# Performance work log

Hardware: AMD Instinct MI355X
Metric: run time of the kernel (lower is better)

The kernel has to match this reference:

```python
import jax, jax.numpy as jnp
import numpy as np

B, N, M = 2, 2048, 1024
C, CTX, H = 1024, 1024, 16
D = C // H
HID = int(C * 4.0)
EPS = 1e-6


def _ln(h):
    # LayerNorm32: fp32 layernorm, eps=1e-6, no affine params
    h32 = h.astype(jnp.float32)
    mu = jnp.mean(h32, axis=-1, keepdims=True)
    var = jnp.var(h32, axis=-1, keepdims=True)
    return ((h32 - mu) * jax.lax.rsqrt(var + EPS)).astype(h.dtype)


def _sdpa(q, k, v):
    # q: [B,Q,H,D], k/v: [B,K,H,D]
    scale = 1.0 / np.sqrt(D)
    s = jnp.einsum('bqhd,bkhd->bhqk', q, k) * scale
    p = jax.nn.softmax(s, axis=-1)
    return jnp.einsum('bhqk,bkhd->bqhd', p, v)


def _forward(x, context, Wqkv, bqkv, Wos, bos, Wq, bq, Wkv, bkv, Woc, boc, W1, b1, W2, b2):
    Bx, Nx, _ = x.shape
    Mx = context.shape[1]
    # --- self-attention (attn_mode='full') ---
    h = _ln(x)
    qkv = (h @ Wqkv + bqkv).reshape(Bx, Nx, 3, H, D)
    q, k, v = qkv[:, :, 0], qkv[:, :, 1], qkv[:, :, 2]
    a = _sdpa(q, k, v).reshape(Bx, Nx, C)
    x = x + (a @ Wos + bos)
    # --- cross-attention (always 'full') ---
    h = _ln(x)
    q = (h @ Wq + bq).reshape(Bx, Nx, H, D)
    kv = (context @ Wkv + bkv).reshape(Bx, Mx, 2, H, D)
    k, v = kv[:, :, 0], kv[:, :, 1]
    a = _sdpa(q, k, v).reshape(Bx, Nx, C)
    x = x + (a @ Woc + boc)
    # --- FFN with tanh-approx GELU ---
    h = _ln(x)
    x = x + (jax.nn.gelu(h @ W1 + b1, approximate=True) @ W2 + b2)
    return x


def setup_inputs() -> dict:
    key = jax.random.key(0)
    ks = jax.random.split(key, 12)
    rn = lambda k, shape: (jax.random.normal(k, shape, jnp.float32) * 0.02)
    return {
        'x': jax.random.normal(ks[0], (B, N, C), jnp.float32),
        'context': jax.random.normal(ks[1], (B, M, CTX), jnp.float32),
        'Wqkv': rn(ks[2], (C, 3 * C)), 'bqkv': jnp.zeros((3 * C,), jnp.float32),
        'Wos': rn(ks[3], (C, C)), 'bos': jnp.zeros((C,), jnp.float32),
        'Wq': rn(ks[4], (C, C)), 'bq': jnp.zeros((C,), jnp.float32),
        'Wkv': rn(ks[5], (CTX, 2 * C)), 'bkv': jnp.zeros((2 * C,), jnp.float32),
        'Woc': rn(ks[6], (C, C)), 'boc': jnp.zeros((C,), jnp.float32),
        'W1': rn(ks[7], (C, HID)), 'b1': jnp.zeros((HID,), jnp.float32),
        'W2': rn(ks[8], (HID, C)), 'b2': jnp.zeros((C,), jnp.float32),
    }


def reference(x, context, Wqkv, bqkv, Wos, bos, Wq, bq, Wkv, bkv, Woc, boc, W1, b1, W2, b2):
    return _forward(x, context, Wqkv, bqkv, Wos, bos, Wq, bq, Wkv, bkv, Woc, boc, W1, b1, W2, b2)
```

## Files before the change

### kernel.cpp

```cpp
#include <hip/hip_runtime.h>
#include <cstdint>

typedef unsigned short u16;
typedef short bf16x8 __attribute__((ext_vector_type(8)));
typedef unsigned short u16x8 __attribute__((ext_vector_type(8)));
typedef float f32x4 __attribute__((ext_vector_type(4)));

__device__ __forceinline__ u16 f2bf(float f) {
  union { float f; uint32_t u; } v; v.f = f;
  uint32_t r = (v.u + 0x7fffu + ((v.u >> 16) & 1u)) >> 16;
  return (u16)r;
}

__device__ __forceinline__ void gload_lds16(const u16* g, u16* l) {
  __builtin_amdgcn_global_load_lds(
      (const __attribute__((address_space(1))) void*)g,
      (__attribute__((address_space(3))) void*)l, 16, 0, 0);
}

__global__ __launch_bounds__(256) void ln_kernel(const float* __restrict__ x,
                                                 u16* __restrict__ h) {
  const int row = blockIdx.x;
  const int tid = threadIdx.x;
  const float4 v = *reinterpret_cast<const float4*>(x + (long)row * 1024 + tid * 4);
  float s  = v.x + v.y + v.z + v.w;
  float ss = v.x * v.x + v.y * v.y + v.z * v.z + v.w * v.w;
#pragma unroll
  for (int off = 32; off >= 1; off >>= 1) {
    s  += __shfl_xor(s, off, 64);
    ss += __shfl_xor(ss, off, 64);
  }
  __shared__ float red[8];
  const int wave = tid >> 6, lane = tid & 63;
  if (lane == 0) { red[wave] = s; red[4 + wave] = ss; }
  __syncthreads();
  s  = red[0] + red[1] + red[2] + red[3];
  ss = red[4] + red[5] + red[6] + red[7];
  const float mu   = s * (1.0f / 1024.0f);
  const float var  = ss * (1.0f / 1024.0f) - mu * mu;
  const float rstd = rsqrtf(var + 1e-6f);
  ushort4 o;
  o.x = f2bf((v.x - mu) * rstd);
  o.y = f2bf((v.y - mu) * rstd);
  o.z = f2bf((v.z - mu) * rstd);
  o.w = f2bf((v.w - mu) * rstd);
  *reinterpret_cast<ushort4*>(h + (long)row * 1024 + tid * 4) = o;
}

struct WEnt { const float* W; u16* Wt; int K, N, tEnd; };
struct WEnts { WEnt e[7]; int n; };

__global__ __launch_bounds__(256) void wconvert_all(WEnts args) {
  __shared__ u16 tile[64][72];
  int t = blockIdx.x;
  int i = 0, tStart = 0;
  while (i < args.n - 1 && t >= args.e[i].tEnd) { tStart = args.e[i].tEnd; i++; }
  const float* W = args.e[i].W;
  u16* Wt = args.e[i].Wt;
  const int K = args.e[i].K, N = args.e[i].N;
  const int rel = t - tStart;
  const int ntn = N >> 6;
  const int tn = rel % ntn, tk = rel / ntn;
  const int n0 = tn * 64, k0 = tk * 64;

  const int th = threadIdx.x;
  const int c4 = (th & 15) * 4;
  const int r  = th >> 4;
#pragma unroll
  for (int ii = 0; ii < 4; ii++) {
    const int row = ii * 16 + r;
    const float4 v = *reinterpret_cast<const float4*>(W + (long)(k0 + row) * N + n0 + c4);
    tile[c4 + 0][row] = f2bf(v.x);
    tile[c4 + 1][row] = f2bf(v.y);
    tile[c4 + 2][row] = f2bf(v.z);
    tile[c4 + 3][row] = f2bf(v.w);
  }
  __syncthreads();
  const int c8 = (th & 7) * 8;
  const int rn = th >> 3;
#pragma unroll
  for (int ii = 0; ii < 2; ii++) {
    const int row = ii * 32 + rn;
    *reinterpret_cast<u16x8*>(Wt + (long)(n0 + row) * K + k0 + c8) =
        *reinterpret_cast<const u16x8*>(&tile[row][c8]);
  }
}

__global__ __launch_bounds__(256) void f2bf_kernel(const float* __restrict__ in,
                                                   u16* __restrict__ out) {
  const long i = ((long)blockIdx.x * 256 + threadIdx.x) * 4;
  const float4 v = *reinterpret_cast<const float4*>(in + i);
  ushort4 o;
  o.x = f2bf(v.x); o.y = f2bf(v.y); o.z = f2bf(v.z); o.w = f2bf(v.w);
  *reinterpret_cast<ushort4*>(out + i) = o;
}

__global__ __launch_bounds__(256) void vtrans(const u16* __restrict__ V,
                                              u16* __restrict__ Vt,
                                              int vStride, long vBatch, int nk) {
  const int tid = threadIdx.x;
  const int b = blockIdx.z, h = blockIdx.y, n0 = blockIdx.x * 64;
  const u16* vp = V + (long)b * vBatch + h * 64;
  u16* op = Vt + (long)(b * 16 + h) * 64 * (long)nk + n0;
  const int d = tid >> 3;
  const int seg = tid & 7;
#pragma unroll
  for (int i = 0; i < 2; i++) {
    const int dd = i * 32 + d;
    u16x8 w;
#pragma unroll
    for (int j = 0; j < 8; j++) w[j] = vp[(long)(n0 + seg * 8 + j) * vStride + dd];
    *reinterpret_cast<u16x8*>(op + (long)dd * nk + seg * 8) = w;
  }
}

template <int TN, bool OUT_BF16, bool GELU_ACT, bool RES>
__global__ __launch_bounds__(256, 2) void gemm_bt(
    const u16* __restrict__ A, const u16* __restrict__ Bt,
    const float* __restrict__ bias, const float* __restrict__ res,
    void* __restrict__ Cout, int Ndim, int Kdim) {
  constexpr int NFRAG = TN / 32;
  __shared__ u16 Al[128 * 32];
  __shared__ u16 Bl[TN * 32];
  const int tid  = threadIdx.x;
  const int lane = tid & 63, wave = tid >> 6;
  const int quad = lane >> 4, l15 = lane & 15;
  const int wr = wave >> 1, wc = wave & 1;
  const int m0 = blockIdx.y * 128, n0 = blockIdx.x * TN;

  f32x4 acc[4][NFRAG];
  const f32x4 vzero = {0.f, 0.f, 0.f, 0.f};
#pragma unroll
  for (int i = 0; i < 4; i++)
#pragma unroll
    for (int j = 0; j < NFRAG; j++) acc[i][j] = vzero;

  const long rowOff = (long)(lane >> 2) * Kdim + (lane & 3) * 8;
  const u16* gA = A  + (long)m0 * Kdim + rowOff;
  const u16* gB = Bt + (long)n0 * Kdim + rowOff;

  for (int k0 = 0; k0 < Kdim; k0 += 32) {
    __syncthreads();
    gload_lds16(gA + (long)(wave * 16) * Kdim + k0,       &Al[wave * 512]);
    gload_lds16(gA + (long)((wave + 4) * 16) * Kdim + k0, &Al[(wave + 4) * 512]);
    gload_lds16(gB + (long)(wave * 16) * Kdim + k0,       &Bl[wave * 512]);
    if constexpr (TN == 128)
      gload_lds16(gB + (long)((wave + 4) * 16) * Kdim + k0, &Bl[(wave + 4) * 512]);
    __syncthreads();

    bf16x8 af[4], bfr[NFRAG];
#pragma unroll
    for (int mt = 0; mt < 4; mt++)
      af[mt] = *reinterpret_cast<const bf16x8*>(&Al[(wr * 64 + mt * 16 + l15) * 32 + quad * 8]);
#pragma unroll
    for (int nt = 0; nt < NFRAG; nt++)
      bfr[nt] = *reinterpret_cast<const bf16x8*>(&Bl[(wc * NFRAG * 16 + nt * 16 + l15) * 32 + quad * 8]);
#pragma unroll
    for (int mt = 0; mt < 4; mt++)
#pragma unroll
      for (int nt = 0; nt < NFRAG; nt++)
        acc[mt][nt] = __builtin_amdgcn_mfma_f32_16x16x32_bf16(af[mt], bfr[nt], acc[mt][nt], 0, 0, 0);
  }

#pragma unroll
  for (int nt = 0; nt < NFRAG; nt++) {
    const int col = n0 + wc * NFRAG * 16 + nt * 16 + l15;
    const float bv = bias[col];
#pragma unroll
    for (int mt = 0; mt < 4; mt++) {
#pragma unroll
      for (int r = 0; r < 4; r++) {
        const int row = m0 + wr * 64 + mt * 16 + quad * 4 + r;
        float y = acc[mt][nt][r] + bv;
        if (GELU_ACT) {
          const float t = 0.7978845608028654f * (y + 0.044715f * y * y * y);
          y = 0.5f * y * (1.0f + tanhf(t));
        }
        if (RES) y += res[(long)row * Ndim + col];
        if (OUT_BF16)
          ((u16*)Cout)[(long)row * Ndim + col] = f2bf(y);
        else
          ((float*)Cout)[(long)row * Ndim + col] = y;
      }
    }
  }
}

__global__ __launch_bounds__(256, 2) void attn_kernel(
    const u16* __restrict__ Q, const u16* __restrict__ K, const u16* __restrict__ Vt,
    u16* __restrict__ O, int nk, int qStride, int kStride, int oStride,
    long qBatch, long kBatch, long oBatch) {
  __shared__ u16 Kt[64 * 64];
  __shared__ u16 Vl[64 * 64];
  __shared__ u16 Pl[4][32 * 64];

  const int tid = threadIdx.x;
  const int lane = tid & 63, wave = tid >> 6;
  const int quad = lane >> 4, l15 = lane & 15;
  const int b = blockIdx.z, hh = blockIdx.y, qt = blockIdx.x;

  const u16* qp = Q + (long)b * qBatch + hh * 64;
  const u16* kp = K + (long)b * kBatch + hh * 64;
  const u16* vp = Vt + (long)(b * 16 + hh) * 64 * (long)nk;

  bf16x8 qf[2][2];
  const int qrow = qt * 128 + wave * 32 + l15;
#pragma unroll
  for (int qg = 0; qg < 2; qg++) {
    qf[qg][0] = *reinterpret_cast<const bf16x8*>(qp + (long)(qrow + qg * 16) * qStride + quad * 8);
    qf[qg][1] = *reinterpret_cast<const bf16x8*>(qp + (long)(qrow + qg * 16) * qStride + 32 + quad * 8);
  }

  const int r8 = lane >> 3;
  const int gcol = ((lane & 7) ^ r8) * 8;
  const u16* kgA = kp + (long)(wave * 8 + r8) * kStride + gcol;
  const u16* kgB = kp + (long)((wave + 4) * 8 + r8) * kStride + gcol;
  const u16* vgA = vp + (long)(wave * 8 + r8) * nk + gcol;
  const u16* vgB = vp + (long)((wave + 4) * 8 + r8) * nk + gcol;

  const int cF = (quad ^ (l15 & 7)) * 8;

  const f32x4 vzero = {0.f, 0.f, 0.f, 0.f};
  f32x4 oAcc[2][4];
  float lSt[2] = {0.f, 0.f};
#pragma unroll
  for (int qg = 0; qg < 2; qg++)
#pragma unroll
    for (int i = 0; i < 4; i++) oAcc[qg][i] = vzero;

  const float SCL = 0.18033688f;
  const int nTiles = nk >> 6;
  const long kAdv = (long)64 * kStride;

  for (int kt = 0; kt < nTiles; kt++) {
    __syncthreads();
    gload_lds16(kgA + kt * kAdv, &Kt[wave * 512]);
    gload_lds16(kgB + kt * kAdv, &Kt[(wave + 4) * 512]);
    gload_lds16(vgA + kt * 64,   &Vl[wave * 512]);
    gload_lds16(vgB + kt * 64,   &Vl[(wave + 4) * 512]);
    __syncthreads();

    f32x4 st[2][4];
#pragma unroll
    for (int mt = 0; mt < 4; mt++) {
      const bf16x8 kf0 = *reinterpret_cast<const bf16x8*>(&Kt[(mt * 16 + l15) * 64 + cF]);
      const bf16x8 kf1 = *reinterpret_cast<const bf16x8*>(&Kt[(mt * 16 + l15) * 64 + (cF ^ 32)]);
#pragma unroll
      for (int qg = 0; qg < 2; qg++) {
        f32x4 z = vzero;
        z = __builtin_amdgcn_mfma_f32_16x16x32_bf16(kf0, qf[qg][0], z, 0, 0, 0);
        z = __builtin_amdgcn_mfma_f32_16x16x32_bf16(kf1, qf[qg][1], z, 0, 0, 0);
        st[qg][mt] = z;
      }
    }

#pragma unroll
    for (int qg = 0; qg < 2; qg++) {
      float ps = 0.f;
#pragma unroll
      for (int mt = 0; mt < 4; mt++)
#pragma unroll
        for (int r = 0; r < 4; r++) {
          const float p = __builtin_amdgcn_exp2f(st[qg][mt][r] * SCL);
          st[qg][mt][r] = p;
          ps += p;
        }
      lSt[qg] += ps;
      u16* plw = &Pl[wave][(qg * 16 + l15) * 64];
#pragma unroll
      for (int mt = 0; mt < 4; mt++) {
        union { float f; uint32_t u; } a0, a1, a2, a3;
        a0.f = st[qg][mt][0]; a1.f = st[qg][mt][1];
        a2.f = st[qg][mt][2]; a3.f = st[qg][mt][3];
        a0.u += 0x8000u; a1.u += 0x8000u; a2.u += 0x8000u; a3.u += 0x8000u;
        uint2 w;
        w.x = __builtin_amdgcn_perm(a1.u, a0.u, 0x07060302u);
        w.y = __builtin_amdgcn_perm(a3.u, a2.u, 0x07060302u);
        const int pcol = (((mt * 2 + (quad >> 1)) ^ (l15 & 7)) * 8) + (quad & 1) * 4;
        *reinterpret_cast<uint2*>(&plw[pcol]) = w;
      }
    }

    bf16x8 pf[2][2];
#pragma unroll
    for (int qg = 0; qg < 2; qg++) {
      const u16* plw = &Pl[wave][(qg * 16 + l15) * 64];
      pf[qg][0] = *reinterpret_cast<const bf16x8*>(&plw[cF]);
      pf[qg][1] = *reinterpret_cast<const bf16x8*>(&plw[cF ^ 32]);
    }
#pragma unroll
    for (int dt = 0; dt < 4; dt++) {
      const bf16x8 vf0 = *reinterpret_cast<const bf16x8*>(&Vl[(dt * 16 + l15) * 64 + cF]);
      const bf16x8 vf1 = *reinterpret_cast<const bf16x8*>(&Vl[(dt * 16 + l15) * 64 + (cF ^ 32)]);
#pragma unroll
      for (int qg = 0; qg < 2; qg++) {
        oAcc[qg][dt] = __builtin_amdgcn_mfma_f32_16x16x32_bf16(pf[qg][0], vf0, oAcc[qg][dt], 0, 0, 0);
        oAcc[qg][dt] = __builtin_amdgcn_mfma_f32_16x16x32_bf16(pf[qg][1], vf1, oAcc[qg][dt], 0, 0, 0);
      }
    }
  }

  u16* op = O + (long)b * oBatch + hh * 64;
#pragma unroll
  for (int qg = 0; qg < 2; qg++) {
    float l = lSt[qg];
    l += __shfl_xor(l, 16, 64);
    l += __shfl_xor(l, 32, 64);
    float lR[4];
#pragma unroll
    for (int r = 0; r < 4; r++) lR[r] = 1.0f / __shfl(l, quad * 4 + r, 64);
#pragma unroll
    for (int dt = 0; dt < 4; dt++)
#pragma unroll
      for (int r = 0; r < 4; r++) {
        const int row = qt * 128 + wave * 32 + qg * 16 + quad * 4 + r;
        op[(long)row * oStride + dt * 16 + l15] = f2bf(oAcc[qg][dt][r] * lR[r]);
      }
  }
}

extern "C" void kernel_launch(void* const* d_in, const int* in_sizes, int n_in,
                              void* d_out, int out_size, void* d_ws, size_t ws_size,
                              hipStream_t stream) {
  const float* x    = (const float*)d_in[0];
  const float* ctx  = (const float*)d_in[1];
  const float* Wqkv = (const float*)d_in[2];
  const float* bqkv = (const float*)d_in[3];
  const float* Wos  = (const float*)d_in[4];
  const float* bos  = (const float*)d_in[5];
  const float* Wq   = (const float*)d_in[6];
  const float* bq   = (const float*)d_in[7];
  const float* Wkv  = (const float*)d_in[8];
  const float* bkv  = (const float*)d_in[9];
  const float* Woc  = (const float*)d_in[10];
  const float* boc  = (const float*)d_in[11];
  const float* W1   = (const float*)d_in[12];
  const float* b1   = (const float*)d_in[13];
  const float* W2   = (const float*)d_in[14];
  const float* b2   = (const float*)d_in[15];
  float* out = (float*)d_out;
  char* ws = (char*)d_ws;
  const size_t MB = 1024 * 1024;

  if (ws_size >= 80 * MB) {
    u16* Wqkvt = (u16*)(ws + 0 * MB);
    u16* Wost  = (u16*)(ws + 6 * MB);
    u16* Wqt   = (u16*)(ws + 8 * MB);
    u16* Wkvt  = (u16*)(ws + 10 * MB);
    u16* Woct  = (u16*)(ws + 14 * MB);
    u16* W1t   = (u16*)(ws + 16 * MB);
    u16* W2t   = (u16*)(ws + 24 * MB);
    u16* h     = (u16*)(ws + 32 * MB);
    u16* abuf  = (u16*)(ws + 40 * MB);
    u16* qkv   = (u16*)(ws + 48 * MB);
    u16* q2    = (u16*)(ws + 48 * MB);
    u16* kv2   = (u16*)(ws + 56 * MB);
    u16* ctxbf = (u16*)(ws + 64 * MB);
    u16* VtCr  = (u16*)(ws + 68 * MB);
    u16* hid   = (u16*)(ws + 48 * MB);
    u16* VtSelf = h;

    WEnts we;
    we.n = 7;
    we.e[0] = {Wqkv, Wqkvt, 1024, 3072, 768};
    we.e[1] = {Wos,  Wost,  1024, 1024, 1024};
    we.e[2] = {Wq,   Wqt,   1024, 1024, 1280};
    we.e[3] = {Wkv,  Wkvt,  1024, 2048, 1792};
    we.e[4] = {Woc,  Woct,  1024, 1024, 2048};
    we.e[5] = {W1,   W1t,   1024, 4096, 3072};
    we.e[6] = {W2,   W2t,   4096, 1024, 4096};
    wconvert_all<<<dim3(4096), dim3(256), 0, stream>>>(we);
    f2bf_kernel<<<dim3(2048), dim3(256), 0, stream>>>(ctx, ctxbf);

    ln_kernel<<<dim3(4096), dim3(256), 0, stream>>>(x, h);
    gemm_bt<128, true, false, false><<<dim3(24, 32), dim3(256), 0, stream>>>(
        h, Wqkvt, bqkv, nullptr, qkv, 3072, 1024);
    vtrans<<<dim3(32, 16, 2), dim3(256), 0, stream>>>(
        qkv + 2048, VtSelf, 3072, (long)2048 * 3072, 2048);
    attn_kernel<<<dim3(16, 16, 2), dim3(256), 0, stream>>>(
        qkv, qkv + 1024, VtSelf, abuf, 2048, 3072, 3072, 1024,
        (long)2048 * 3072, (long)2048 * 3072, (long)2048 * 1024);
    gemm_bt<64, false, false, true><<<dim3(16, 32), dim3(256), 0, stream>>>(
        abuf, Wost, bos, x, out, 1024, 1024);
    ln_kernel<<<dim3(4096), dim3(256), 0, stream>>>(out, h);
    gemm_bt<64, true, false, false><<<dim3(16, 32), dim3(256), 0, stream>>>(
        h, Wqt, bq, nullptr, q2, 1024, 1024);
    gemm_bt<64, true, false, false><<<dim3(32, 16), dim3(256), 0, stream>>>(
        ctxbf, Wkvt, bkv, nullptr, kv2, 2048, 1024);
    vtrans<<<dim3(16, 16, 2), dim3(256), 0, stream>>>(
        kv2 + 1024, VtCr, 2048, (long)1024 * 2048, 1024);
    attn_kernel<<<dim3(16, 16, 2), dim3(256), 0, stream>>>(
        q2, kv2, VtCr, abuf, 1024, 1024, 2048, 1024,
        (long)2048 * 1024, (long)1024 * 2048, (long)2048 * 1024);
    gemm_bt<64, false, false, true><<<dim3(16, 32), dim3(256), 0, stream>>>(
        abuf, Woct, boc, out, out, 1024, 1024);
    ln_kernel<<<dim3(4096), dim3(256), 0, stream>>>(out, h);
    gemm_bt<128, true, true, false><<<dim3(32, 32), dim3(256), 0, stream>>>(
        h, W1t, b1, nullptr, hid, 4096, 1024);
    gemm_bt<64, false, false, true><<<dim3(16, 32), dim3(256), 0, stream>>>(
        hid, W2t, b2, out, out, 1024, 4096);
  } else {
    u16* h      = (u16*)ws;
    u16* wbuf   = (u16*)(ws + 8 * MB);
    char* C0    = ws + 16 * MB;
    u16* qkv    = (u16*)C0;
    u16* Wqkvt  = (u16*)(C0 + 24 * MB);
    u16* Wost   = (u16*)C0;
    u16* q2     = (u16*)C0;
    u16* kv2    = (u16*)(C0 + 8 * MB);
    u16* Wqt    = (u16*)(C0 + 16 * MB);
    u16* Wkvt   = (u16*)(C0 + 16 * MB);
    u16* ctxbf  = (u16*)(C0 + 20 * MB);
    u16* VtCr   = (u16*)(C0 + 24 * MB);
    u16* Woct   = (u16*)(C0 + 16 * MB);
    u16* hid    = (u16*)C0;
    u16* VtSelf = h;
    u16* abuf   = wbuf;
    u16* W1t    = wbuf;
    u16* W2t    = wbuf;
    WEnts w1; w1.n = 1;

    ln_kernel<<<dim3(4096), dim3(256), 0, stream>>>(x, h);
    w1.e[0] = {Wqkv, Wqkvt, 1024, 3072, 768};
    wconvert_all<<<dim3(768), dim3(256), 0, stream>>>(w1);
    gemm_bt<128, true, false, false><<<dim3(24, 32), dim3(256), 0, stream>>>(
        h, Wqkvt, bqkv, nullptr, qkv, 3072, 1024);
    vtrans<<<dim3(32, 16, 2), dim3(256), 0, stream>>>(
        qkv + 2048, VtSelf, 3072, (long)2048 * 3072, 2048);
    attn_kernel<<<dim3(16, 16, 2), dim3(256), 0, stream>>>(
        qkv, qkv + 1024, VtSelf, abuf, 2048, 3072, 3072, 1024,
        (long)2048 * 3072, (long)2048 * 3072, (long)2048 * 1024);
    w1.e[0] = {Wos, Wost, 1024, 1024, 256};
    wconvert_all<<<dim3(256), dim3(256), 0, stream>>>(w1);
    gemm_bt<64, false, false, true><<<dim3(16, 32), dim3(256), 0, stream>>>(
        abuf, Wost, bos, x, out, 1024, 1024);
    ln_kernel<<<dim3(4096), dim3(256), 0, stream>>>(out, h);
    w1.e[0] = {Wq, Wqt, 1024, 1024, 256};
    wconvert_all<<<dim3(256), dim3(256), 0, stream>>>(w1);
    gemm_bt<64, true, false, false><<<dim3(16, 32), dim3(256), 0, stream>>>(
        h, Wqt, bq, nullptr, q2, 1024, 1024);
    f2bf_kernel<<<dim3(2048), dim3(256), 0, stream>>>(ctx, ctxbf);
    w1.e[0] = {Wkv, Wkvt, 1024, 2048, 512};
    wconvert_all<<<dim3(512), dim3(256), 0, stream>>>(w1);
    gemm_bt<64, true, false, false><<<dim3(32, 16), dim3(256), 0, stream>>>(
        ctxbf, Wkvt, bkv, nullptr, kv2, 2048, 1024);
    vtrans<<<dim3(16, 16, 2), dim3(256), 0, stream>>>(
        kv2 + 1024, VtCr, 2048, (long)1024 * 2048, 1024);
    attn_kernel<<<dim3(16, 16, 2), dim3(256), 0, stream>>>(
        q2, kv2, VtCr, abuf, 1024, 1024, 2048, 1024,
        (long)2048 * 1024, (long)1024 * 2048, (long)2048 * 1024);
    w1.e[0] = {Woc, Woct, 1024, 1024, 256};
    wconvert_all<<<dim3(256), dim3(256), 0, stream>>>(w1);
    gemm_bt<64, false, false, true><<<dim3(16, 32), dim3(256), 0, stream>>>(
        abuf, Woct, boc, out, out, 1024, 1024);
    ln_kernel<<<dim3(4096), dim3(256), 0, stream>>>(out, h);
    w1.e[0] = {W1, W1t, 1024, 4096, 1024};
    wconvert_all<<<dim3(1024), dim3(256), 0, stream>>>(w1);
    gemm_bt<128, true, true, false><<<dim3(32, 32), dim3(256), 0, stream>>>(
        h, W1t, b1, nullptr, hid, 4096, 1024);
    w1.e[0] = {W2, W2t, 4096, 1024, 1024};
    wconvert_all<<<dim3(1024), dim3(256), 0, stream>>>(w1);
    gemm_bt<64, false, false, true><<<dim3(16, 32), dim3(256), 0, stream>>>(
        hid, W2t, b2, out, out, 1024, 4096);
  }
}
```

Baseline: 508.6 us.

## Remap GEMM blocks to XCD-local tile groups and transpose V through LDS

The GEMM grid becomes 1D, and block indices are remapped so that each of the 8 XCDs (blocks assigned round-robin by j&7) gets a contiguous 2D region of output tiles. Neighbouring tiles then share A/B panels in that XCD's L2. The V transpose kernel now uses coalesced 16-byte row loads into an LDS tile and 16-byte stores, replacing strided scalar gathers. The price is extra index arithmetic, and correctness depends on the lx/ly/SX parameters exactly tiling each grid.

```diff
diff --git a/kernel.cpp b/kernel.cpp
--- a/kernel.cpp
+++ b/kernel.cpp
@@ -98,42 +98,54 @@
 __global__ __launch_bounds__(256) void vtrans(const u16* __restrict__ V,
                                               u16* __restrict__ Vt,
                                               int vStride, long vBatch, int nk) {
-  const int tid = threadIdx.x;
+  __shared__ u16 tile[64][72];
+  const int t = threadIdx.x;
   const int b = blockIdx.z, h = blockIdx.y, n0 = blockIdx.x * 64;
   const u16* vp = V + (long)b * vBatch + h * 64;
   u16* op = Vt + (long)(b * 16 + h) * 64 * (long)nk + n0;
-  const int d = tid >> 3;
-  const int seg = tid & 7;
+  const int ch = t & 7;
 #pragma unroll
   for (int i = 0; i < 2; i++) {
-    const int dd = i * 32 + d;
-    u16x8 w;
-#pragma unroll
-    for (int j = 0; j < 8; j++) w[j] = vp[(long)(n0 + seg * 8 + j) * vStride + dd];
-    *reinterpret_cast<u16x8*>(op + (long)dd * nk + seg * 8) = w;
-  }
-}
-
-template <int TN, bool OUT_BF16, bool GELU_ACT, bool RES>
+    const int n = (t >> 3) + i * 32;
+    const u16x8 v = *reinterpret_cast<const u16x8*>(vp + (long)(n0 + n) * vStride + ch * 8);
+#pragma unroll
+    for (int j = 0; j < 8; j++) tile[ch * 8 + j][n] = v[j];
+  }
+  __syncthreads();
+#pragma unroll
+  for (int i = 0; i < 2; i++) {
+    const int d = (t >> 3) + i * 32;
+    *reinterpret_cast<u16x8*>(op + (long)d * nk + ch * 8) =
+        *reinterpret_cast<const u16x8*>(&tile[d][ch * 8]);
+  }
+}
+
+template <int TN, int SX, bool OUT_BF16, bool GELU_ACT, bool RES>
 __global__ __launch_bounds__(256, 2) void gemm_bt(
     const u16* __restrict__ A, const u16* __restrict__ Bt,
     const float* __restrict__ bias, const float* __restrict__ res,
-    void* __restrict__ Cout, int Ndim, int Kdim) {
+    void* __restrict__ Cout, int Ndim, int Kdim, int lx, int ly) {
   constexpr int NFRAG = TN / 32;
   __shared__ u16 Al[128 * 32];
   __shared__ u16 Bl[TN * 32];
+  const int j = blockIdx.x;
+  const int c = j & 7, kk = j >> 3;
+  const int cx = c % SX, cy = c / SX;
+  const int bx = cx * lx + (kk % lx);
+  const int by = cy * ly + (kk / lx);
+  const int m0 = by * 128, n0 = bx * TN;
+
   const int tid  = threadIdx.x;
   const int lane = tid & 63, wave = tid >> 6;
   const int quad = lane >> 4, l15 = lane & 15;
   const int wr = wave >> 1, wc = wave & 1;
-  const int m0 = blockIdx.y * 128, n0 = blockIdx.x * TN;
 
   f32x4 acc[4][NFRAG];
   const f32x4 vzero = {0.f, 0.f, 0.f, 0.f};
 #pragma unroll
   for (int i = 0; i < 4; i++)
 #pragma unroll
-    for (int j = 0; j < NFRAG; j++) acc[i][j] = vzero;
+    for (int jj = 0; jj < NFRAG; jj++) acc[i][jj] = vzero;
 
   const long rowOff = (long)(lane >> 2) * Kdim + (lane & 3) * 8;
   const u16* gA = A  + (long)m0 * Kdim + rowOff;
@@ -373,32 +385,32 @@
     f2bf_kernel<<<dim3(2048), dim3(256), 0, stream>>>(ctx, ctxbf);
 
     ln_kernel<<<dim3(4096), dim3(256), 0, stream>>>(x, h);
-    gemm_bt<128, true, false, false><<<dim3(24, 32), dim3(256), 0, stream>>>(
-        h, Wqkvt, bqkv, nullptr, qkv, 3072, 1024);
+    gemm_bt<128, 2, true, false, false><<<dim3(768), dim3(256), 0, stream>>>(
+        h, Wqkvt, bqkv, nullptr, qkv, 3072, 1024, 12, 8);
     vtrans<<<dim3(32, 16, 2), dim3(256), 0, stream>>>(
         qkv + 2048, VtSelf, 3072, (long)2048 * 3072, 2048);
     attn_kernel<<<dim3(16, 16, 2), dim3(256), 0, stream>>>(
         qkv, qkv + 1024, VtSelf, abuf, 2048, 3072, 3072, 1024,
         (long)2048 * 3072, (long)2048 * 3072, (long)2048 * 1024);
-    gemm_bt<64, false, false, true><<<dim3(16, 32), dim3(256), 0, stream>>>(
-        abuf, Wost, bos, x, out, 1024, 1024);
+    gemm_bt<64, 1, false, false, true><<<dim3(512), dim3(256), 0, stream>>>(
+        abuf, Wost, bos, x, out, 1024, 1024, 16, 4);
     ln_kernel<<<dim3(4096), dim3(256), 0, stream>>>(out, h);
-    gemm_bt<64, true, false, false><<<dim3(16, 32), dim3(256), 0, stream>>>(
-        h, Wqt, bq, nullptr, q2, 1024, 1024);
-    gemm_bt<64, true, false, false><<<dim3(32, 16), dim3(256), 0, stream>>>(
-        ctxbf, Wkvt, bkv, nullptr, kv2, 2048, 1024);
+    gemm_bt<64, 1, true, false, false><<<dim3(512), dim3(256), 0, stream>>>(
+        h, Wqt, bq, nullptr, q2, 1024, 1024, 16, 4);
+    gemm_bt<64, 2, true, false, false><<<dim3(512), dim3(256), 0, stream>>>(
+        ctxbf, Wkvt, bkv, nullptr, kv2, 2048, 1024, 16, 4);
     vtrans<<<dim3(16, 16, 2), dim3(256), 0, stream>>>(
         kv2 + 1024, VtCr, 2048, (long)1024 * 2048, 1024);
     attn_kernel<<<dim3(16, 16, 2), dim3(256), 0, stream>>>(
         q2, kv2, VtCr, abuf, 1024, 1024, 2048, 1024,
         (long)2048 * 1024, (long)1024 * 2048, (long)2048 * 1024);
-    gemm_bt<64, false, false, true><<<dim3(16, 32), dim3(256), 0, stream>>>(
-        abuf, Woct, boc, out, out, 1024, 1024);
+    gemm_bt<64, 1, false, false, true><<<dim3(512), dim3(256), 0, stream>>>(
+        abuf, Woct, boc, out, out, 1024, 1024, 16, 4);
     ln_kernel<<<dim3(4096), dim3(256), 0, stream>>>(out, h);
-    gemm_bt<128, true, true, false><<<dim3(32, 32), dim3(256), 0, stream>>>(
-        h, W1t, b1, nullptr, hid, 4096, 1024);
-    gemm_bt<64, false, false, true><<<dim3(16, 32), dim3(256), 0, stream>>>(
-        hid, W2t, b2, out, out, 1024, 4096);
+    gemm_bt<128, 2, true, true, false><<<dim3(1024), dim3(256), 0, stream>>>(
+        h, W1t, b1, nullptr, hid, 4096, 1024, 16, 8);
+    gemm_bt<64, 2, false, false, true><<<dim3(512), dim3(256), 0, stream>>>(
+        hid, W2t, b2, out, out, 1024, 4096, 8, 8);
   } else {
     u16* h      = (u16*)ws;
     u16* wbuf   = (u16*)(ws + 8 * MB);
@@ -423,8 +435,8 @@
     ln_kernel<<<dim3(4096), dim3(256), 0, stream>>>(x, h);
     w1.e[0] = {Wqkv, Wqkvt, 1024, 3072, 768};
     wconvert_all<<<dim3(768), dim3(256), 0, stream>>>(w1);
-    gemm_bt<128, true, false, false><<<dim3(24, 32), dim3(256), 0, stream>>>(
-        h, Wqkvt, bqkv, nullptr, qkv, 3072, 1024);
+    gemm_bt<128, 2, true, false, false><<<dim3(768), dim3(256), 0, stream>>>(
+        h, Wqkvt, bqkv, nullptr, qkv, 3072, 1024, 12, 8);
     vtrans<<<dim3(32, 16, 2), dim3(256), 0, stream>>>(
         qkv + 2048, VtSelf, 3072, (long)2048 * 3072, 2048);
     attn_kernel<<<dim3(16, 16, 2), dim3(256), 0, stream>>>(
@@ -432,18 +444,18 @@
         (long)2048 * 3072, (long)2048 * 3072, (long)2048 * 1024);
     w1.e[0] = {Wos, Wost, 1024, 1024, 256};
     wconvert_all<<<dim3(256), dim3(256), 0, stream>>>(w1);
-    gemm_bt<64, false, false, true><<<dim3(16, 32), dim3(256), 0, stream>>>(
-        abuf, Wost, bos, x, out, 1024, 1024);
+    gemm_bt<64, 1, false, false, true><<<dim3(512), dim3(256), 0, stream>>>(
+        abuf, Wost, bos, x, out, 1024, 1024, 16, 4);
     ln_kernel<<<dim3(4096), dim3(256), 0, stream>>>(out, h);
     w1.e[0] = {Wq, Wqt, 1024, 1024, 256};
     wconvert_all<<<dim3(256), dim3(256), 0, stream>>>(w1);
-    gemm_bt<64, true, false, false><<<dim3(16, 32), dim3(256), 0, stream>>>(
-        h, Wqt, bq, nullptr, q2, 1024, 1024);
+    gemm_bt<64, 1, true, false, false><<<dim3(512), dim3(256), 0, stream>>>(
+        h, Wqt, bq, nullptr, q2, 1024, 1024, 16, 4);
     f2bf_kernel<<<dim3(2048), dim3(256), 0, stream>>>(ctx, ctxbf);
     w1.e[0] = {Wkv, Wkvt, 1024, 2048, 512};
     wconvert_all<<<dim3(512), dim3(256), 0, stream>>>(w1);
-    gemm_bt<64, true, false, false><<<dim3(32, 16), dim3(256), 0, stream>>>(
-        ctxbf, Wkvt, bkv, nullptr, kv2, 2048, 1024);
+    gemm_bt<64, 2, true, false, false><<<dim3(512), dim3(256), 0, stream>>>(
+        ctxbf, Wkvt, bkv, nullptr, kv2, 2048, 1024, 16, 4);
     vtrans<<<dim3(16, 16, 2), dim3(256), 0, stream>>>(
         kv2 + 1024, VtCr, 2048, (long)1024 * 2048, 1024);
     attn_kernel<<<dim3(16, 16, 2), dim3(256), 0, stream>>>(
@@ -451,16 +463,16 @@
         (long)2048 * 1024, (long)1024 * 2048, (long)2048 * 1024);
     w1.e[0] = {Woc, Woct, 1024, 1024, 256};
     wconvert_all<<<dim3(256), dim3(256), 0, stream>>>(w1);
-    gemm_bt<64, false, false, true><<<dim3(16, 32), dim3(256), 0, stream>>>(
-        abuf, Woct, boc, out, out, 1024, 1024);
+    gemm_bt<64, 1, false, false, true><<<dim3(512), dim3(256), 0, stream>>>(
+        abuf, Woct, boc, out, out, 1024, 1024, 16, 4);
     ln_kernel<<<dim3(4096), dim3(256), 0, stream>>>(out, h);
     w1.e[0] = {W1, W1t, 1024, 4096, 1024};
     wconvert_all<<<dim3(1024), dim3(256), 0, stream>>>(w1);
-    gemm_bt<128, true, true, false><<<dim3(32, 32), dim3(256), 0, stream>>>(
-        h, W1t, b1, nullptr, hid, 4096, 1024);
+    gemm_bt<128, 2, true, true, false><<<dim3(1024), dim3(256), 0, stream>>>(
+        h, W1t, b1, nullptr, hid, 4096, 1024, 16, 8);
     w1.e[0] = {W2, W2t, 4096, 1024, 1024};
     wconvert_all<<<dim3(1024), dim3(256), 0, stream>>>(w1);
-    gemm_bt<64, false, false, true><<<dim3(16, 32), dim3(256), 0, stream>>>(
-        hid, W2t, b2, out, out, 1024, 4096);
-  }
-}
+    gemm_bt<64, 2, false, false, true><<<dim3(512), dim3(256), 0, stream>>>(
+        hid, W2t, b2, out, out, 1024, 4096, 8, 8);
+  }
+}
```

Result: faster. 495.3 us (-2.6%).
